# Kernel tuning notes

Measured on AMD Instinct MI355X. Metric: run time of the kernel, lower is better.

## Reference

```python
import jax, jax.numpy as jnp
import numpy as np

B = 100000          # polymers
MOLS_PER = 4        # 3 monomers + 1 solvent per polymer
N = B * MOLS_PER
D = 64              # rdkit feature dim
F = 64              # polymer-level feature dim
H = 128             # hidden dim


def setup_inputs() -> dict:
    key = jax.random.key(0)
    ks = jax.random.split(key, 6)
    polymer_feats = jax.random.normal(ks[0], (B, F), dtype=jnp.float32)
    rdkit = jax.random.normal(ks[1], (N, D), dtype=jnp.float32)
    # sorted segment ids; last molecule of each segment is the solvent
    polymer_mapping = jnp.repeat(jnp.arange(B, dtype=jnp.int32), MOLS_PER)
    W1 = jax.random.normal(ks[2], (F + 2 * D, H), dtype=jnp.float32) * 0.05
    b1 = jnp.zeros((H,), jnp.float32)
    W2 = jax.random.normal(ks[3], (H, H // 2), dtype=jnp.float32) * 0.05
    b2 = jnp.zeros((H // 2,), jnp.float32)
    W3 = jax.random.normal(ks[4], (H // 2, 1), dtype=jnp.float32) * 0.05
    b3 = jnp.zeros((1,), jnp.float32)
    return {"polymer_feats": polymer_feats, "rdkit": rdkit,
            "polymer_mapping": polymer_mapping,
            "W1": W1, "b1": b1, "W2": W2, "b2": b2, "W3": W3, "b3": b3}


def _combine_rdkit(rdkit, polymer_mapping, num_polymers):
    # solvent = last row of each consecutive segment
    last = jnp.concatenate([polymer_mapping[1:] != polymer_mapping[:-1],
                            jnp.ones((1,), dtype=bool)])
    mono = ~last
    mono_w = mono.astype(rdkit.dtype)
    mono_sum = jax.ops.segment_sum(rdkit * mono_w[:, None], polymer_mapping,
                                   num_segments=num_polymers)
    mono_cnt = jax.ops.segment_sum(mono_w, polymer_mapping,
                                   num_segments=num_polymers)
    mono_avg = mono_sum / mono_cnt[:, None]
    solvent = jax.ops.segment_sum(rdkit * last.astype(rdkit.dtype)[:, None],
                                  polymer_mapping, num_segments=num_polymers)
    return jnp.concatenate([mono_avg, solvent], axis=1)  # [B, 2D]


def reference(polymer_feats, rdkit, polymer_mapping, W1, b1, W2, b2, W3, b3):
    num_polymers = polymer_feats.shape[0]
    pooled = _combine_rdkit(rdkit, polymer_mapping, num_polymers)
    x = jnp.concatenate([polymer_feats, pooled], axis=1)  # [B, F+2D]
    h = jax.nn.relu(x @ W1 + b1)          # dropout is identity in eval mode
    h = jax.nn.relu(h @ W2 + b2)
    return h @ W3 + b3                    # [B, 1]
```

## Files before the change

kernel.cpp:

```cpp
#include <hip/hip_runtime.h>

#define BPOLY  100000
#define TILE_M 64
#define NBLK   ((BPOLY + TILE_M - 1) / TILE_M)
#define KSTR   200

typedef __attribute__((ext_vector_type(8))) _Float16 f16x8;
typedef __attribute__((ext_vector_type(4))) _Float16 f16x4;
typedef __attribute__((ext_vector_type(4))) float    f32x4;

#define W1T 0
#define W2T 24576

__global__ __launch_bounds__(256) void prep_weights(
    const float* __restrict__ W1,
    const float* __restrict__ W2,
    _Float16* __restrict__ ws) {
  int i = blockIdx.x * 256 + threadIdx.x;
  if (i < 24576) {
    int k = i >> 7, n = i & 127;
    ws[W1T + n * 192 + k] = (_Float16)W1[i];
  } else {
    int j = i - 24576;
    int k = j >> 6, n = j & 63;
    ws[W2T + n * 128 + k] = (_Float16)W2[j];
  }
}

__global__ __launch_bounds__(256, 6) void fnn_mfma(
    const float* __restrict__ pf,
    const float* __restrict__ rdkit,
    const _Float16* __restrict__ ws,
    const float* __restrict__ b1,
    const float* __restrict__ b2,
    const float* __restrict__ W3,
    const float* __restrict__ b3,
    float* __restrict__ out) {
  __shared__ __align__(16) _Float16 Xs[64 * KSTR];

  const int tid  = threadIdx.x;
  const int p0   = blockIdx.x * TILE_M;
  const int lane = tid & 63;
  const int wv   = tid >> 6;
  const int lmod = lane & 15;
  const int lq   = lane >> 4;

  #pragma unroll
  for (int i = 0; i < 4; ++i) {
    int f = tid + i * 256;
    int m = f >> 4, kq = (f & 15) * 4;
    float4 v = make_float4(0.f, 0.f, 0.f, 0.f);
    if (p0 + m < BPOLY) v = *(const float4*)(pf + (size_t)(p0 + m) * 64 + kq);
    f16x4 h = {(_Float16)v.x, (_Float16)v.y, (_Float16)v.z, (_Float16)v.w};
    *(f16x4*)&Xs[m * KSTR + kq] = h;
  }
  #pragma unroll
  for (int i = 0; i < 4; ++i) {
    int f = tid + i * 256;
    int m = f >> 4, kq = (f & 15) * 4;
    float4 r0 = {0,0,0,0}, r1 = {0,0,0,0}, r2 = {0,0,0,0}, r3 = {0,0,0,0};
    if (p0 + m < BPOLY) {
      const float* base = rdkit + (size_t)(p0 + m) * 256 + kq;
      r0 = *(const float4*)(base);
      r1 = *(const float4*)(base + 64);
      r2 = *(const float4*)(base + 128);
      r3 = *(const float4*)(base + 192);
    }
    const float inv3 = 1.0f / 3.0f;
    f16x4 av = {(_Float16)((r0.x + r1.x + r2.x) * inv3),
                (_Float16)((r0.y + r1.y + r2.y) * inv3),
                (_Float16)((r0.z + r1.z + r2.z) * inv3),
                (_Float16)((r0.w + r1.w + r2.w) * inv3)};
    f16x4 sv = {(_Float16)r3.x, (_Float16)r3.y, (_Float16)r3.z, (_Float16)r3.w};
    *(f16x4*)&Xs[m * KSTR + 64 + kq]  = av;
    *(f16x4*)&Xs[m * KSTR + 128 + kq] = sv;
  }
  __syncthreads();

  const float b1v0 = b1[32 * wv + lmod];
  const float b1v1 = b1[32 * wv + 16 + lmod];
  const _Float16* w1t = ws + W1T;
  const int bcol0 = (32 * wv + lmod) * 192;
  const int bcol1 = (32 * wv + 16 + lmod) * 192;

  f32x4 acc1[4][2];
  #pragma unroll
  for (int mt = 0; mt < 4; ++mt) {
    acc1[mt][0] = (f32x4){0.f, 0.f, 0.f, 0.f};
    acc1[mt][1] = (f32x4){0.f, 0.f, 0.f, 0.f};
  }

  #pragma unroll 2
  for (int ks = 0; ks < 6; ++ks) {
    const int ko = ks * 32 + lq * 8;
    f16x8 b0 = *(const f16x8*)(w1t + bcol0 + ko);
    f16x8 b1f = *(const f16x8*)(w1t + bcol1 + ko);
    #pragma unroll
    for (int mt = 0; mt < 4; ++mt) {
      f16x8 a = *(const f16x8*)&Xs[(mt * 16 + lmod) * KSTR + ko];
      acc1[mt][0] = __builtin_amdgcn_mfma_f32_16x16x32_f16(a, b0,  acc1[mt][0], 0, 0, 0);
      acc1[mt][1] = __builtin_amdgcn_mfma_f32_16x16x32_f16(a, b1f, acc1[mt][1], 0, 0, 0);
    }
  }
  __syncthreads();

  #pragma unroll
  for (int mt = 0; mt < 4; ++mt) {
    #pragma unroll
    for (int nn = 0; nn < 2; ++nn) {
      const float bv = nn ? b1v1 : b1v0;
      const int col = 32 * wv + 16 * nn + lmod;
      #pragma unroll
      for (int r = 0; r < 4; ++r) {
        float h = fmaxf(acc1[mt][nn][r] + bv, 0.f);
        Xs[(mt * 16 + lq * 4 + r) * KSTR + col] = (_Float16)h;
      }
    }
  }
  __syncthreads();

  const float b2v = b2[16 * wv + lmod];
  const float w3v = W3[16 * wv + lmod];
  const _Float16* w2t = ws + W2T;
  const int bcol2 = (16 * wv + lmod) * 128;

  f32x4 acc2[4];
  #pragma unroll
  for (int mt = 0; mt < 4; ++mt) acc2[mt] = (f32x4){0.f, 0.f, 0.f, 0.f};

  #pragma unroll 2
  for (int ks = 0; ks < 4; ++ks) {
    const int ko = ks * 32 + lq * 8;
    f16x8 b = *(const f16x8*)(w2t + bcol2 + ko);
    #pragma unroll
    for (int mt = 0; mt < 4; ++mt) {
      f16x8 a = *(const f16x8*)&Xs[(mt * 16 + lmod) * KSTR + ko];
      acc2[mt] = __builtin_amdgcn_mfma_f32_16x16x32_f16(a, b, acc2[mt], 0, 0, 0);
    }
  }

  float part[4][4];
  #pragma unroll
  for (int mt = 0; mt < 4; ++mt)
    #pragma unroll
    for (int r = 0; r < 4; ++r)
      part[mt][r] = fmaxf(acc2[mt][r] + b2v, 0.f) * w3v;

  #pragma unroll
  for (int mask = 1; mask <= 8; mask <<= 1)
    #pragma unroll
    for (int mt = 0; mt < 4; ++mt)
      #pragma unroll
      for (int r = 0; r < 4; ++r)
        part[mt][r] += __shfl_xor(part[mt][r], mask);

  if (lmod == 0) {
    #pragma unroll
    for (int mt = 0; mt < 4; ++mt)
      #pragma unroll
      for (int r = 0; r < 4; ++r) {
        int row = mt * 16 + lq * 4 + r;
        *(float*)&Xs[row * KSTR + 128 + 2 * wv] = part[mt][r];
      }
  }
  __syncthreads();

  if (tid < 64) {
    int p = p0 + tid;
    if (p < BPOLY) {
      float4 ps = *(const float4*)&Xs[tid * KSTR + 128];
      out[p] = ps.x + ps.y + ps.z + ps.w + b3[0];
    }
  }
}

extern "C" void kernel_launch(void* const* d_in, const int* in_sizes, int n_in,
                              void* d_out, int out_size, void* d_ws, size_t ws_size,
                              hipStream_t stream) {
  const float* pf    = (const float*)d_in[0];
  const float* rdkit = (const float*)d_in[1];
  const float* W1 = (const float*)d_in[3];
  const float* b1 = (const float*)d_in[4];
  const float* W2 = (const float*)d_in[5];
  const float* b2 = (const float*)d_in[6];
  const float* W3 = (const float*)d_in[7];
  const float* b3 = (const float*)d_in[8];
  _Float16* ws = (_Float16*)d_ws;
  float* out = (float*)d_out;

  prep_weights<<<128, 256, 0, stream>>>(W1, W2, ws);
  fnn_mfma<<<NBLK, 256, 0, stream>>>(pf, rdkit, ws, b1, b2, W3, b3, out);
}
```

Before: 195.4 us.

## Process two tiles per block and prefetch second tile during first GEMM

Each block now handles two 64-row tiles using two shared-memory buffers. The global loads for the second tile are issued into registers before the first tile's layer-1 MFMA loop and committed to LDS afterwards, so memory latency can hide behind compute. Grid size halves and occupancy hint drops from 6 to 3 blocks per CU. The cost is doubled LDS use and many more live registers, which may reduce latency hiding across waves.

```diff
diff --git a/kernel.cpp b/kernel.cpp
--- a/kernel.cpp
+++ b/kernel.cpp
@@ -2,7 +2,8 @@
 
 #define BPOLY  100000
 #define TILE_M 64
-#define NBLK   ((BPOLY + TILE_M - 1) / TILE_M)
+#define NTILE  1564
+#define NBLK   (NTILE / 2)
 #define KSTR   200
 
 typedef __attribute__((ext_vector_type(8))) _Float16 f16x8;
@@ -27,7 +28,58 @@
   }
 }
 
-__global__ __launch_bounds__(256, 6) void fnn_mfma(
+struct StagedTile {
+  float4 pfv[4];
+  float4 rk[4][4];
+};
+
+__device__ __forceinline__ void stage_issue(const float* __restrict__ pf,
+                                            const float* __restrict__ rdkit,
+                                            int p0, int tid, StagedTile& s) {
+  #pragma unroll
+  for (int i = 0; i < 4; ++i) {
+    int f = tid + i * 256, m = f >> 4, kq = (f & 15) * 4;
+    float4 z = {0.f, 0.f, 0.f, 0.f};
+    s.pfv[i] = (p0 + m < BPOLY) ? *(const float4*)(pf + (size_t)(p0 + m) * 64 + kq) : z;
+  }
+  #pragma unroll
+  for (int i = 0; i < 4; ++i) {
+    int f = tid + i * 256, m = f >> 4, kq = (f & 15) * 4;
+    float4 z = {0.f, 0.f, 0.f, 0.f};
+    const float* base = rdkit + (size_t)(p0 + m) * 256 + kq;
+    bool ok = (p0 + m < BPOLY);
+    s.rk[i][0] = ok ? *(const float4*)(base)       : z;
+    s.rk[i][1] = ok ? *(const float4*)(base + 64)  : z;
+    s.rk[i][2] = ok ? *(const float4*)(base + 128) : z;
+    s.rk[i][3] = ok ? *(const float4*)(base + 192) : z;
+  }
+}
+
+__device__ __forceinline__ void stage_commit(_Float16* __restrict__ Xs, int tid,
+                                             const StagedTile& s) {
+  #pragma unroll
+  for (int i = 0; i < 4; ++i) {
+    int f = tid + i * 256, m = f >> 4, kq = (f & 15) * 4;
+    float4 v = s.pfv[i];
+    f16x4 h = {(_Float16)v.x, (_Float16)v.y, (_Float16)v.z, (_Float16)v.w};
+    *(f16x4*)&Xs[m * KSTR + kq] = h;
+  }
+  #pragma unroll
+  for (int i = 0; i < 4; ++i) {
+    int f = tid + i * 256, m = f >> 4, kq = (f & 15) * 4;
+    float4 r0 = s.rk[i][0], r1 = s.rk[i][1], r2 = s.rk[i][2], r3 = s.rk[i][3];
+    const float inv3 = 1.0f / 3.0f;
+    f16x4 av = {(_Float16)((r0.x + r1.x + r2.x) * inv3),
+                (_Float16)((r0.y + r1.y + r2.y) * inv3),
+                (_Float16)((r0.z + r1.z + r2.z) * inv3),
+                (_Float16)((r0.w + r1.w + r2.w) * inv3)};
+    f16x4 sv = {(_Float16)r3.x, (_Float16)r3.y, (_Float16)r3.z, (_Float16)r3.w};
+    *(f16x4*)&Xs[m * KSTR + 64 + kq]  = av;
+    *(f16x4*)&Xs[m * KSTR + 128 + kq] = sv;
+  }
+}
+
+__global__ __launch_bounds__(256, 3) void fnn_mfma(
     const float* __restrict__ pf,
     const float* __restrict__ rdkit,
     const _Float16* __restrict__ ws,
@@ -36,52 +88,36 @@
     const float* __restrict__ W3,
     const float* __restrict__ b3,
     float* __restrict__ out) {
-  __shared__ __align__(16) _Float16 Xs[64 * KSTR];
+  __shared__ __align__(16) _Float16 Xs0[64 * KSTR];
+  __shared__ __align__(16) _Float16 Xs1[64 * KSTR];
 
   const int tid  = threadIdx.x;
-  const int p0   = blockIdx.x * TILE_M;
   const int lane = tid & 63;
   const int wv   = tid >> 6;
   const int lmod = lane & 15;
   const int lq   = lane >> 4;
 
-  #pragma unroll
-  for (int i = 0; i < 4; ++i) {
-    int f = tid + i * 256;
-    int m = f >> 4, kq = (f & 15) * 4;
-    float4 v = make_float4(0.f, 0.f, 0.f, 0.f);
-    if (p0 + m < BPOLY) v = *(const float4*)(pf + (size_t)(p0 + m) * 64 + kq);
-    f16x4 h = {(_Float16)v.x, (_Float16)v.y, (_Float16)v.z, (_Float16)v.w};
-    *(f16x4*)&Xs[m * KSTR + kq] = h;
-  }
-  #pragma unroll
-  for (int i = 0; i < 4; ++i) {
-    int f = tid + i * 256;
-    int m = f >> 4, kq = (f & 15) * 4;
-    float4 r0 = {0,0,0,0}, r1 = {0,0,0,0}, r2 = {0,0,0,0}, r3 = {0,0,0,0};
-    if (p0 + m < BPOLY) {
-      const float* base = rdkit + (size_t)(p0 + m) * 256 + kq;
-      r0 = *(const float4*)(base);
-      r1 = *(const float4*)(base + 64);
-      r2 = *(const float4*)(base + 128);
-      r3 = *(const float4*)(base + 192);
-    }
-    const float inv3 = 1.0f / 3.0f;
-    f16x4 av = {(_Float16)((r0.x + r1.x + r2.x) * inv3),
-                (_Float16)((r0.y + r1.y + r2.y) * inv3),
-                (_Float16)((r0.z + r1.z + r2.z) * inv3),
-                (_Float16)((r0.w + r1.w + r2.w) * inv3)};
-    f16x4 sv = {(_Float16)r3.x, (_Float16)r3.y, (_Float16)r3.z, (_Float16)r3.w};
-    *(f16x4*)&Xs[m * KSTR + 64 + kq]  = av;
-    *(f16x4*)&Xs[m * KSTR + 128 + kq] = sv;
-  }
-  __syncthreads();
+  const int p0a = (blockIdx.x * 2) * TILE_M;
+  const int p0b = (blockIdx.x * 2 + 1) * TILE_M;
 
   const float b1v0 = b1[32 * wv + lmod];
   const float b1v1 = b1[32 * wv + 16 + lmod];
+  const float b2v  = b2[16 * wv + lmod];
+  const float w3v  = W3[16 * wv + lmod];
+  const float b3v  = b3[0];
+
   const _Float16* w1t = ws + W1T;
+  const _Float16* w2t = ws + W2T;
   const int bcol0 = (32 * wv + lmod) * 192;
   const int bcol1 = (32 * wv + 16 + lmod) * 192;
+  const int bcol2 = (16 * wv + lmod) * 128;
+
+  StagedTile st;
+  stage_issue(pf, rdkit, p0a, tid, st);
+  stage_commit(Xs0, tid, st);
+  __syncthreads();
+
+  stage_issue(pf, rdkit, p0b, tid, st);
 
   f32x4 acc1[4][2];
   #pragma unroll
@@ -89,23 +125,24 @@
     acc1[mt][0] = (f32x4){0.f, 0.f, 0.f, 0.f};
     acc1[mt][1] = (f32x4){0.f, 0.f, 0.f, 0.f};
   }
-
   #pragma unroll 2
   for (int ks = 0; ks < 6; ++ks) {
     const int ko = ks * 32 + lq * 8;
-    f16x8 b0 = *(const f16x8*)(w1t + bcol0 + ko);
-    f16x8 b1f = *(const f16x8*)(w1t + bcol1 + ko);
+    f16x8 w0 = *(const f16x8*)(w1t + bcol0 + ko);
+    f16x8 w1 = *(const f16x8*)(w1t + bcol1 + ko);
     #pragma unroll
     for (int mt = 0; mt < 4; ++mt) {
-      f16x8 a = *(const f16x8*)&Xs[(mt * 16 + lmod) * KSTR + ko];
-      acc1[mt][0] = __builtin_amdgcn_mfma_f32_16x16x32_f16(a, b0,  acc1[mt][0], 0, 0, 0);
-      acc1[mt][1] = __builtin_amdgcn_mfma_f32_16x16x32_f16(a, b1f, acc1[mt][1], 0, 0, 0);
-    }
-  }
-  __syncthreads();
-
-  #pragma unroll
-  for (int mt = 0; mt < 4; ++mt) {
+      f16x8 a = *(const f16x8*)&Xs0[(mt * 16 + lmod) * KSTR + ko];
+      acc1[mt][0] = __builtin_amdgcn_mfma_f32_16x16x32_f16(a, w0, acc1[mt][0], 0, 0, 0);
+      acc1[mt][1] = __builtin_amdgcn_mfma_f32_16x16x32_f16(a, w1, acc1[mt][1], 0, 0, 0);
+    }
+  }
+
+  stage_commit(Xs1, tid, st);
+  __syncthreads();
+
+  #pragma unroll
+  for (int mt = 0; mt < 4; ++mt)
     #pragma unroll
     for (int nn = 0; nn < 2; ++nn) {
       const float bv = nn ? b1v1 : b1v0;
@@ -113,63 +150,131 @@
       #pragma unroll
       for (int r = 0; r < 4; ++r) {
         float h = fmaxf(acc1[mt][nn][r] + bv, 0.f);
-        Xs[(mt * 16 + lq * 4 + r) * KSTR + col] = (_Float16)h;
-      }
-    }
-  }
-  __syncthreads();
-
-  const float b2v = b2[16 * wv + lmod];
-  const float w3v = W3[16 * wv + lmod];
-  const _Float16* w2t = ws + W2T;
-  const int bcol2 = (16 * wv + lmod) * 128;
-
-  f32x4 acc2[4];
-  #pragma unroll
-  for (int mt = 0; mt < 4; ++mt) acc2[mt] = (f32x4){0.f, 0.f, 0.f, 0.f};
-
+        Xs0[(mt * 16 + lq * 4 + r) * KSTR + col] = (_Float16)h;
+      }
+    }
+  __syncthreads();
+
+  {
+    f32x4 acc2[4];
+    #pragma unroll
+    for (int mt = 0; mt < 4; ++mt) acc2[mt] = (f32x4){0.f, 0.f, 0.f, 0.f};
+    #pragma unroll 2
+    for (int ks = 0; ks < 4; ++ks) {
+      const int ko = ks * 32 + lq * 8;
+      f16x8 w = *(const f16x8*)(w2t + bcol2 + ko);
+      #pragma unroll
+      for (int mt = 0; mt < 4; ++mt) {
+        f16x8 a = *(const f16x8*)&Xs0[(mt * 16 + lmod) * KSTR + ko];
+        acc2[mt] = __builtin_amdgcn_mfma_f32_16x16x32_f16(a, w, acc2[mt], 0, 0, 0);
+      }
+    }
+    float part[4][4];
+    #pragma unroll
+    for (int mt = 0; mt < 4; ++mt)
+      #pragma unroll
+      for (int r = 0; r < 4; ++r)
+        part[mt][r] = fmaxf(acc2[mt][r] + b2v, 0.f) * w3v;
+    #pragma unroll
+    for (int mask = 1; mask <= 8; mask <<= 1)
+      #pragma unroll
+      for (int mt = 0; mt < 4; ++mt)
+        #pragma unroll
+        for (int r = 0; r < 4; ++r)
+          part[mt][r] += __shfl_xor(part[mt][r], mask);
+    if (lmod == 0) {
+      #pragma unroll
+      for (int mt = 0; mt < 4; ++mt)
+        #pragma unroll
+        for (int r = 0; r < 4; ++r)
+          *(float*)&Xs0[(mt * 16 + lq * 4 + r) * KSTR + 128 + 2 * wv] = part[mt][r];
+    }
+  }
+  __syncthreads();
+
+  if (tid < 64) {
+    int p = p0a + tid;
+    if (p < BPOLY) {
+      float4 ps = *(const float4*)&Xs0[tid * KSTR + 128];
+      out[p] = ps.x + ps.y + ps.z + ps.w + b3v;
+    }
+  }
+
+  #pragma unroll
+  for (int mt = 0; mt < 4; ++mt) {
+    acc1[mt][0] = (f32x4){0.f, 0.f, 0.f, 0.f};
+    acc1[mt][1] = (f32x4){0.f, 0.f, 0.f, 0.f};
+  }
   #pragma unroll 2
-  for (int ks = 0; ks < 4; ++ks) {
+  for (int ks = 0; ks < 6; ++ks) {
     const int ko = ks * 32 + lq * 8;
-    f16x8 b = *(const f16x8*)(w2t + bcol2 + ko);
+    f16x8 w0 = *(const f16x8*)(w1t + bcol0 + ko);
+    f16x8 w1 = *(const f16x8*)(w1t + bcol1 + ko);
     #pragma unroll
     for (int mt = 0; mt < 4; ++mt) {
-      f16x8 a = *(const f16x8*)&Xs[(mt * 16 + lmod) * KSTR + ko];
-      acc2[mt] = __builtin_amdgcn_mfma_f32_16x16x32_f16(a, b, acc2[mt], 0, 0, 0);
-    }
-  }
-
-  float part[4][4];
+      f16x8 a = *(const f16x8*)&Xs1[(mt * 16 + lmod) * KSTR + ko];
+      acc1[mt][0] = __builtin_amdgcn_mfma_f32_16x16x32_f16(a, w0, acc1[mt][0], 0, 0, 0);
+      acc1[mt][1] = __builtin_amdgcn_mfma_f32_16x16x32_f16(a, w1, acc1[mt][1], 0, 0, 0);
+    }
+  }
+  __syncthreads();
+
   #pragma unroll
   for (int mt = 0; mt < 4; ++mt)
     #pragma unroll
-    for (int r = 0; r < 4; ++r)
-      part[mt][r] = fmaxf(acc2[mt][r] + b2v, 0.f) * w3v;
-
-  #pragma unroll
-  for (int mask = 1; mask <= 8; mask <<= 1)
+    for (int nn = 0; nn < 2; ++nn) {
+      const float bv = nn ? b1v1 : b1v0;
+      const int col = 32 * wv + 16 * nn + lmod;
+      #pragma unroll
+      for (int r = 0; r < 4; ++r) {
+        float h = fmaxf(acc1[mt][nn][r] + bv, 0.f);
+        Xs1[(mt * 16 + lq * 4 + r) * KSTR + col] = (_Float16)h;
+      }
+    }
+  __syncthreads();
+
+  {
+    f32x4 acc2[4];
+    #pragma unroll
+    for (int mt = 0; mt < 4; ++mt) acc2[mt] = (f32x4){0.f, 0.f, 0.f, 0.f};
+    #pragma unroll 2
+    for (int ks = 0; ks < 4; ++ks) {
+      const int ko = ks * 32 + lq * 8;
+      f16x8 w = *(const f16x8*)(w2t + bcol2 + ko);
+      #pragma unroll
+      for (int mt = 0; mt < 4; ++mt) {
+        f16x8 a = *(const f16x8*)&Xs1[(mt * 16 + lmod) * KSTR + ko];
+        acc2[mt] = __builtin_amdgcn_mfma_f32_16x16x32_f16(a, w, acc2[mt], 0, 0, 0);
+      }
+    }
+    float part[4][4];
     #pragma unroll
     for (int mt = 0; mt < 4; ++mt)
       #pragma unroll
       for (int r = 0; r < 4; ++r)
-        part[mt][r] += __shfl_xor(part[mt][r], mask);
-
-  if (lmod == 0) {
-    #pragma unroll
-    for (int mt = 0; mt < 4; ++mt)
-      #pragma unroll
-      for (int r = 0; r < 4; ++r) {
-        int row = mt * 16 + lq * 4 + r;
-        *(float*)&Xs[row * KSTR + 128 + 2 * wv] = part[mt][r];
-      }
+        part[mt][r] = fmaxf(acc2[mt][r] + b2v, 0.f) * w3v;
+    #pragma unroll
+    for (int mask = 1; mask <= 8; mask <<= 1)
+      #pragma unroll
+      for (int mt = 0; mt < 4; ++mt)
+        #pragma unroll
+        for (int r = 0; r < 4; ++r)
+          part[mt][r] += __shfl_xor(part[mt][r], mask);
+    if (lmod == 0) {
+      #pragma unroll
+      for (int mt = 0; mt < 4; ++mt)
+        #pragma unroll
+        for (int r = 0; r < 4; ++r)
+          *(float*)&Xs1[(mt * 16 + lq * 4 + r) * KSTR + 128 + 2 * wv] = part[mt][r];
+    }
   }
   __syncthreads();
 
   if (tid < 64) {
-    int p = p0 + tid;
+    int p = p0b + tid;
     if (p < BPOLY) {
-      float4 ps = *(const float4*)&Xs[tid * KSTR + 128];
-      out[p] = ps.x + ps.y + ps.z + ps.w + b3[0];
+      float4 ps = *(const float4*)&Xs1[tid * KSTR + 128];
+      out[p] = ps.x + ps.y + ps.z + ps.w + b3v;
     }
   }
 }
```

Result: slower. 223.0 us (+14.1%).

## Make each wave own 16 polymers, loading A-fragments directly from global memory

Applied to the files above, without the earlier changes.

Restructures the fused MLP so each wavefront independently processes 16 polymers and computes all 128 hidden columns. A fragments are built directly in registers from global fp32 loads, with the monomer average computed in place, instead of staging a 64-row tile in shared memory. Only a small per-wave hidden buffer in LDS is kept, all block-level barriers are removed, and occupancy hints are raised. The trade-off is that each wave now reads all of W1/W2 from global or cache, giving more weight traffic per polymer, and the global loads of rdkit are less coalesced.

```diff
diff --git a/kernel.cpp b/kernel.cpp
--- a/kernel.cpp
+++ b/kernel.cpp
@@ -1,12 +1,11 @@
 #include <hip/hip_runtime.h>
 
 #define BPOLY  100000
-#define TILE_M 64
-#define NBLK   ((BPOLY + TILE_M - 1) / TILE_M)
-#define KSTR   200
+#define NWAVE  6250
+#define NBLK   1563
+#define HSTR   136
 
 typedef __attribute__((ext_vector_type(8))) _Float16 f16x8;
-typedef __attribute__((ext_vector_type(4))) _Float16 f16x4;
 typedef __attribute__((ext_vector_type(4))) float    f32x4;
 
 #define W1T 0
@@ -27,7 +26,14 @@
   }
 }
 
-__global__ __launch_bounds__(256, 6) void fnn_mfma(
+__device__ __forceinline__ f16x8 cvt8(float4 u, float4 v) {
+  f16x8 r;
+  r[0] = (_Float16)u.x; r[1] = (_Float16)u.y; r[2] = (_Float16)u.z; r[3] = (_Float16)u.w;
+  r[4] = (_Float16)v.x; r[5] = (_Float16)v.y; r[6] = (_Float16)v.z; r[7] = (_Float16)v.w;
+  return r;
+}
+
+__global__ __launch_bounds__(256, 8) void fnn_wave(
     const float* __restrict__ pf,
     const float* __restrict__ rdkit,
     const _Float16* __restrict__ ws,
@@ -36,141 +42,108 @@
     const float* __restrict__ W3,
     const float* __restrict__ b3,
     float* __restrict__ out) {
-  __shared__ __align__(16) _Float16 Xs[64 * KSTR];
+  __shared__ __align__(16) _Float16 Hs[4 * 16 * HSTR];
 
   const int tid  = threadIdx.x;
-  const int p0   = blockIdx.x * TILE_M;
+  const int wv   = tid >> 6;
   const int lane = tid & 63;
-  const int wv   = tid >> 6;
   const int lmod = lane & 15;
   const int lq   = lane >> 4;
 
+  const int p0 = (blockIdx.x * 4 + wv) * 16;
+  if (p0 >= BPOLY) return;
+  const int p = p0 + lmod;
+
+  const float4* pf4 = (const float4*)(pf + (size_t)p * 64);
+  const float4* rk4 = (const float4*)(rdkit + (size_t)p * 256);
+
+  const _Float16* w1t = ws + W1T;
+  const _Float16* w2t = ws + W2T;
+
+  f32x4 acc[8];
   #pragma unroll
-  for (int i = 0; i < 4; ++i) {
-    int f = tid + i * 256;
-    int m = f >> 4, kq = (f & 15) * 4;
-    float4 v = make_float4(0.f, 0.f, 0.f, 0.f);
-    if (p0 + m < BPOLY) v = *(const float4*)(pf + (size_t)(p0 + m) * 64 + kq);
-    f16x4 h = {(_Float16)v.x, (_Float16)v.y, (_Float16)v.z, (_Float16)v.w};
-    *(f16x4*)&Xs[m * KSTR + kq] = h;
-  }
+  for (int nt = 0; nt < 8; ++nt) acc[nt] = (f32x4){0.f, 0.f, 0.f, 0.f};
+
   #pragma unroll
-  for (int i = 0; i < 4; ++i) {
-    int f = tid + i * 256;
-    int m = f >> 4, kq = (f & 15) * 4;
-    float4 r0 = {0,0,0,0}, r1 = {0,0,0,0}, r2 = {0,0,0,0}, r3 = {0,0,0,0};
-    if (p0 + m < BPOLY) {
-      const float* base = rdkit + (size_t)(p0 + m) * 256 + kq;
-      r0 = *(const float4*)(base);
-      r1 = *(const float4*)(base + 64);
-      r2 = *(const float4*)(base + 128);
-      r3 = *(const float4*)(base + 192);
+  for (int ks = 0; ks < 6; ++ks) {
+    f16x8 a;
+    if (ks < 2) {
+      int q = ks * 8 + lq * 2;
+      a = cvt8(pf4[q], pf4[q + 1]);
+    } else if (ks < 4) {
+      int q = (ks - 2) * 8 + lq * 2;
+      float4 u0 = rk4[q],      u1 = rk4[q + 1];
+      float4 v0 = rk4[16 + q], v1 = rk4[16 + q + 1];
+      float4 w0 = rk4[32 + q], w1 = rk4[32 + q + 1];
+      const float inv3 = 1.0f / 3.0f;
+      float4 s0 = {(u0.x + v0.x + w0.x) * inv3, (u0.y + v0.y + w0.y) * inv3,
+                   (u0.z + v0.z + w0.z) * inv3, (u0.w + v0.w + w0.w) * inv3};
+      float4 s1 = {(u1.x + v1.x + w1.x) * inv3, (u1.y + v1.y + w1.y) * inv3,
+                   (u1.z + v1.z + w1.z) * inv3, (u1.w + v1.w + w1.w) * inv3};
+      a = cvt8(s0, s1);
+    } else {
+      int q = (ks - 4) * 8 + lq * 2;
+      a = cvt8(rk4[48 + q], rk4[48 + q + 1]);
     }
-    const float inv3 = 1.0f / 3.0f;
-    f16x4 av = {(_Float16)((r0.x + r1.x + r2.x) * inv3),
-                (_Float16)((r0.y + r1.y + r2.y) * inv3),
-                (_Float16)((r0.z + r1.z + r2.z) * inv3),
-                (_Float16)((r0.w + r1.w + r2.w) * inv3)};
-    f16x4 sv = {(_Float16)r3.x, (_Float16)r3.y, (_Float16)r3.z, (_Float16)r3.w};
-    *(f16x4*)&Xs[m * KSTR + 64 + kq]  = av;
-    *(f16x4*)&Xs[m * KSTR + 128 + kq] = sv;
-  }
-  __syncthreads();
-
-  const float b1v0 = b1[32 * wv + lmod];
-  const float b1v1 = b1[32 * wv + 16 + lmod];
-  const _Float16* w1t = ws + W1T;
-  const int bcol0 = (32 * wv + lmod) * 192;
-  const int bcol1 = (32 * wv + 16 + lmod) * 192;
-
-  f32x4 acc1[4][2];
-  #pragma unroll
-  for (int mt = 0; mt < 4; ++mt) {
-    acc1[mt][0] = (f32x4){0.f, 0.f, 0.f, 0.f};
-    acc1[mt][1] = (f32x4){0.f, 0.f, 0.f, 0.f};
+    const int ko = ks * 32 + lq * 8;
+    #pragma unroll
+    for (int nt = 0; nt < 8; ++nt) {
+      f16x8 b = *(const f16x8*)(w1t + (nt * 16 + lmod) * 192 + ko);
+      acc[nt] = __builtin_amdgcn_mfma_f32_16x16x32_f16(a, b, acc[nt], 0, 0, 0);
+    }
   }
 
-  #pragma unroll 2
-  for (int ks = 0; ks < 6; ++ks) {
-    const int ko = ks * 32 + lq * 8;
-    f16x8 b0 = *(const f16x8*)(w1t + bcol0 + ko);
-    f16x8 b1f = *(const f16x8*)(w1t + bcol1 + ko);
+  _Float16* hw = Hs + wv * (16 * HSTR);
+  #pragma unroll
+  for (int nt = 0; nt < 8; ++nt) {
+    float b1c = b1[nt * 16 + lmod];
     #pragma unroll
-    for (int mt = 0; mt < 4; ++mt) {
-      f16x8 a = *(const f16x8*)&Xs[(mt * 16 + lmod) * KSTR + ko];
-      acc1[mt][0] = __builtin_amdgcn_mfma_f32_16x16x32_f16(a, b0,  acc1[mt][0], 0, 0, 0);
-      acc1[mt][1] = __builtin_amdgcn_mfma_f32_16x16x32_f16(a, b1f, acc1[mt][1], 0, 0, 0);
+    for (int r = 0; r < 4; ++r) {
+      float h = fmaxf(acc[nt][r] + b1c, 0.f);
+      hw[(lq * 4 + r) * HSTR + nt * 16 + lmod] = (_Float16)h;
     }
   }
-  __syncthreads();
-
-  #pragma unroll
-  for (int mt = 0; mt < 4; ++mt) {
-    #pragma unroll
-    for (int nn = 0; nn < 2; ++nn) {
-      const float bv = nn ? b1v1 : b1v0;
-      const int col = 32 * wv + 16 * nn + lmod;
-      #pragma unroll
-      for (int r = 0; r < 4; ++r) {
-        float h = fmaxf(acc1[mt][nn][r] + bv, 0.f);
-        Xs[(mt * 16 + lq * 4 + r) * KSTR + col] = (_Float16)h;
-      }
-    }
-  }
-  __syncthreads();
-
-  const float b2v = b2[16 * wv + lmod];
-  const float w3v = W3[16 * wv + lmod];
-  const _Float16* w2t = ws + W2T;
-  const int bcol2 = (16 * wv + lmod) * 128;
+  asm volatile("s_waitcnt lgkmcnt(0)" ::: "memory");
+  __builtin_amdgcn_sched_barrier(0);
 
   f32x4 acc2[4];
   #pragma unroll
-  for (int mt = 0; mt < 4; ++mt) acc2[mt] = (f32x4){0.f, 0.f, 0.f, 0.f};
+  for (int nt = 0; nt < 4; ++nt) acc2[nt] = (f32x4){0.f, 0.f, 0.f, 0.f};
 
-  #pragma unroll 2
+  const _Float16* hrow = hw + lmod * HSTR;
+  #pragma unroll
   for (int ks = 0; ks < 4; ++ks) {
     const int ko = ks * 32 + lq * 8;
-    f16x8 b = *(const f16x8*)(w2t + bcol2 + ko);
+    f16x8 a2 = *(const f16x8*)(hrow + ko);
     #pragma unroll
-    for (int mt = 0; mt < 4; ++mt) {
-      f16x8 a = *(const f16x8*)&Xs[(mt * 16 + lmod) * KSTR + ko];
-      acc2[mt] = __builtin_amdgcn_mfma_f32_16x16x32_f16(a, b, acc2[mt], 0, 0, 0);
+    for (int nt = 0; nt < 4; ++nt) {
+      f16x8 b = *(const f16x8*)(w2t + (nt * 16 + lmod) * 128 + ko);
+      acc2[nt] = __builtin_amdgcn_mfma_f32_16x16x32_f16(a2, b, acc2[nt], 0, 0, 0);
     }
   }
 
-  float part[4][4];
+  float s0 = 0.f, s1 = 0.f, s2 = 0.f, s3 = 0.f;
   #pragma unroll
-  for (int mt = 0; mt < 4; ++mt)
-    #pragma unroll
-    for (int r = 0; r < 4; ++r)
-      part[mt][r] = fmaxf(acc2[mt][r] + b2v, 0.f) * w3v;
-
+  for (int nt = 0; nt < 4; ++nt) {
+    float b2c = b2[nt * 16 + lmod];
+    float w3c = W3[nt * 16 + lmod];
+    s0 = fmaf(fmaxf(acc2[nt][0] + b2c, 0.f), w3c, s0);
+    s1 = fmaf(fmaxf(acc2[nt][1] + b2c, 0.f), w3c, s1);
+    s2 = fmaf(fmaxf(acc2[nt][2] + b2c, 0.f), w3c, s2);
+    s3 = fmaf(fmaxf(acc2[nt][3] + b2c, 0.f), w3c, s3);
+  }
   #pragma unroll
-  for (int mask = 1; mask <= 8; mask <<= 1)
-    #pragma unroll
-    for (int mt = 0; mt < 4; ++mt)
-      #pragma unroll
-      for (int r = 0; r < 4; ++r)
-        part[mt][r] += __shfl_xor(part[mt][r], mask);
+  for (int mask = 1; mask <= 8; mask <<= 1) {
+    s0 += __shfl_xor(s0, mask);
+    s1 += __shfl_xor(s1, mask);
+    s2 += __shfl_xor(s2, mask);
+    s3 += __shfl_xor(s3, mask);
+  }
 
   if (lmod == 0) {
-    #pragma unroll
-    for (int mt = 0; mt < 4; ++mt)
-      #pragma unroll
-      for (int r = 0; r < 4; ++r) {
-        int row = mt * 16 + lq * 4 + r;
-        *(float*)&Xs[row * KSTR + 128 + 2 * wv] = part[mt][r];
-      }
-  }
-  __syncthreads();
-
-  if (tid < 64) {
-    int p = p0 + tid;
-    if (p < BPOLY) {
-      float4 ps = *(const float4*)&Xs[tid * KSTR + 128];
-      out[p] = ps.x + ps.y + ps.z + ps.w + b3[0];
-    }
+    float bb = b3[0];
+    float4 o = {s0 + bb, s1 + bb, s2 + bb, s3 + bb};
+    *(float4*)(out + p0 + lq * 4) = o;
   }
 }
 
@@ -189,5 +162,5 @@
   float* out = (float*)d_out;
 
   prep_weights<<<128, 256, 0, stream>>>(W1, W2, ws);
-  fnn_mfma<<<NBLK, 256, 0, stream>>>(pf, rdkit, ws, b1, b2, W3, b3, out);
+  fnn_wave<<<NBLK, 256, 0, stream>>>(pf, rdkit, ws, b1, b2, W3, b3, out);
 }
```

Result: slower. 234.2 us (+19.9%).

## Fold monomer averaging into W1 and feed MFMA directly from global loads

Applied to the files above, without the earlier changes.

Expands W1 to K=320 by replicating the monomer block three times, prescaled by 1/3, so the mean pooling becomes part of the first GEMM. Activations are then loaded straight from global memory into MFMA operand registers, and the LDS staging of the input tile plus one barrier are removed. This trades more MFMA work (10 k-steps instead of 6) and redundant global loads across the four waves for less LDS traffic and fewer synchronisations. Occupancy hint drops from 6 to 5 blocks.

```diff
diff --git a/kernel.cpp b/kernel.cpp
--- a/kernel.cpp
+++ b/kernel.cpp
@@ -3,31 +3,41 @@
 #define BPOLY  100000
 #define TILE_M 64
 #define NBLK   ((BPOLY + TILE_M - 1) / TILE_M)
-#define KSTR   200
+#define HSTR   136
 
 typedef __attribute__((ext_vector_type(8))) _Float16 f16x8;
-typedef __attribute__((ext_vector_type(4))) _Float16 f16x4;
 typedef __attribute__((ext_vector_type(4))) float    f32x4;
 
-#define W1T 0
-#define W2T 24576
+#define W1T2 0
+#define W2T2 40960
 
 __global__ __launch_bounds__(256) void prep_weights(
     const float* __restrict__ W1,
     const float* __restrict__ W2,
     _Float16* __restrict__ ws) {
   int i = blockIdx.x * 256 + threadIdx.x;
-  if (i < 24576) {
-    int k = i >> 7, n = i & 127;
-    ws[W1T + n * 192 + k] = (_Float16)W1[i];
+  if (i < 40960) {
+    int n = i / 320, k = i % 320;
+    float s;
+    if (k < 64)       s = W1[k * 128 + n];
+    else if (k < 256) s = W1[(64 + ((k - 64) & 63)) * 128 + n] * (1.0f / 3.0f);
+    else              s = W1[(k - 128) * 128 + n];
+    ws[W1T2 + n * 320 + k] = (_Float16)s;
   } else {
-    int j = i - 24576;
+    int j = i - 40960;
     int k = j >> 6, n = j & 63;
-    ws[W2T + n * 128 + k] = (_Float16)W2[j];
+    ws[W2T2 + n * 128 + k] = (_Float16)W2[j];
   }
 }
 
-__global__ __launch_bounds__(256, 6) void fnn_mfma(
+__device__ __forceinline__ f16x8 cvt8(float4 u, float4 v) {
+  f16x8 r;
+  r[0] = (_Float16)u.x; r[1] = (_Float16)u.y; r[2] = (_Float16)u.z; r[3] = (_Float16)u.w;
+  r[4] = (_Float16)v.x; r[5] = (_Float16)v.y; r[6] = (_Float16)v.z; r[7] = (_Float16)v.w;
+  return r;
+}
+
+__global__ __launch_bounds__(256, 5) void fnn_direct(
     const float* __restrict__ pf,
     const float* __restrict__ rdkit,
     const _Float16* __restrict__ ws,
@@ -36,52 +46,28 @@
     const float* __restrict__ W3,
     const float* __restrict__ b3,
     float* __restrict__ out) {
-  __shared__ __align__(16) _Float16 Xs[64 * KSTR];
+  __shared__ __align__(16) _Float16 Hs[64 * HSTR];
+  __shared__ float Psum[4][64];
 
   const int tid  = threadIdx.x;
-  const int p0   = blockIdx.x * TILE_M;
+  const int wv   = tid >> 6;
   const int lane = tid & 63;
-  const int wv   = tid >> 6;
   const int lmod = lane & 15;
   const int lq   = lane >> 4;
 
+  const int p0 = blockIdx.x * TILE_M;
+
+  int pm[4];
   #pragma unroll
-  for (int i = 0; i < 4; ++i) {
-    int f = tid + i * 256;
-    int m = f >> 4, kq = (f & 15) * 4;
-    float4 v = make_float4(0.f, 0.f, 0.f, 0.f);
-    if (p0 + m < BPOLY) v = *(const float4*)(pf + (size_t)(p0 + m) * 64 + kq);
-    f16x4 h = {(_Float16)v.x, (_Float16)v.y, (_Float16)v.z, (_Float16)v.w};
-    *(f16x4*)&Xs[m * KSTR + kq] = h;
+  for (int mt = 0; mt < 4; ++mt) {
+    int p = p0 + mt * 16 + lmod;
+    pm[mt] = p < BPOLY ? p : (BPOLY - 1);
   }
-  #pragma unroll
-  for (int i = 0; i < 4; ++i) {
-    int f = tid + i * 256;
-    int m = f >> 4, kq = (f & 15) * 4;
-    float4 r0 = {0,0,0,0}, r1 = {0,0,0,0}, r2 = {0,0,0,0}, r3 = {0,0,0,0};
-    if (p0 + m < BPOLY) {
-      const float* base = rdkit + (size_t)(p0 + m) * 256 + kq;
-      r0 = *(const float4*)(base);
-      r1 = *(const float4*)(base + 64);
-      r2 = *(const float4*)(base + 128);
-      r3 = *(const float4*)(base + 192);
-    }
-    const float inv3 = 1.0f / 3.0f;
-    f16x4 av = {(_Float16)((r0.x + r1.x + r2.x) * inv3),
-                (_Float16)((r0.y + r1.y + r2.y) * inv3),
-                (_Float16)((r0.z + r1.z + r2.z) * inv3),
-                (_Float16)((r0.w + r1.w + r2.w) * inv3)};
-    f16x4 sv = {(_Float16)r3.x, (_Float16)r3.y, (_Float16)r3.z, (_Float16)r3.w};
-    *(f16x4*)&Xs[m * KSTR + 64 + kq]  = av;
-    *(f16x4*)&Xs[m * KSTR + 128 + kq] = sv;
-  }
-  __syncthreads();
 
-  const float b1v0 = b1[32 * wv + lmod];
-  const float b1v1 = b1[32 * wv + 16 + lmod];
-  const _Float16* w1t = ws + W1T;
-  const int bcol0 = (32 * wv + lmod) * 192;
-  const int bcol1 = (32 * wv + 16 + lmod) * 192;
+  const _Float16* w1t = ws + W1T2;
+  const _Float16* w2t = ws + W2T2;
+  const int n0 = 32 * wv + lmod;
+  const int n1 = n0 + 16;
 
   f32x4 acc1[4][2];
   #pragma unroll
@@ -90,22 +76,34 @@
     acc1[mt][1] = (f32x4){0.f, 0.f, 0.f, 0.f};
   }
 
-  #pragma unroll 2
-  for (int ks = 0; ks < 6; ++ks) {
-    const int ko = ks * 32 + lq * 8;
-    f16x8 b0 = *(const f16x8*)(w1t + bcol0 + ko);
-    f16x8 b1f = *(const f16x8*)(w1t + bcol1 + ko);
+  #pragma unroll
+  for (int ks = 0; ks < 10; ++ks) {
+    const int reg = ks >> 1;
+    const int off = ((ks & 1) << 5) + lq * 8;
+    float4 a0[4], a1[4];
     #pragma unroll
     for (int mt = 0; mt < 4; ++mt) {
-      f16x8 a = *(const f16x8*)&Xs[(mt * 16 + lmod) * KSTR + ko];
-      acc1[mt][0] = __builtin_amdgcn_mfma_f32_16x16x32_f16(a, b0,  acc1[mt][0], 0, 0, 0);
-      acc1[mt][1] = __builtin_amdgcn_mfma_f32_16x16x32_f16(a, b1f, acc1[mt][1], 0, 0, 0);
+      const float* src = (reg == 0)
+          ? pf + (size_t)pm[mt] * 64 + off
+          : rdkit + ((size_t)pm[mt] * 4 + (reg - 1)) * 64 + off;
+      a0[mt] = *(const float4*)(src);
+      a1[mt] = *(const float4*)(src + 4);
+    }
+    const int ko = ks * 32 + lq * 8;
+    f16x8 w0 = *(const f16x8*)(w1t + n0 * 320 + ko);
+    f16x8 w1 = *(const f16x8*)(w1t + n1 * 320 + ko);
+    #pragma unroll
+    for (int mt = 0; mt < 4; ++mt) {
+      f16x8 a = cvt8(a0[mt], a1[mt]);
+      acc1[mt][0] = __builtin_amdgcn_mfma_f32_16x16x32_f16(a, w0, acc1[mt][0], 0, 0, 0);
+      acc1[mt][1] = __builtin_amdgcn_mfma_f32_16x16x32_f16(a, w1, acc1[mt][1], 0, 0, 0);
     }
   }
-  __syncthreads();
 
+  const float b1v0 = b1[n0];
+  const float b1v1 = b1[n1];
   #pragma unroll
-  for (int mt = 0; mt < 4; ++mt) {
+  for (int mt = 0; mt < 4; ++mt)
     #pragma unroll
     for (int nn = 0; nn < 2; ++nn) {
       const float bv = nn ? b1v1 : b1v0;
@@ -113,32 +111,29 @@
       #pragma unroll
       for (int r = 0; r < 4; ++r) {
         float h = fmaxf(acc1[mt][nn][r] + bv, 0.f);
-        Xs[(mt * 16 + lq * 4 + r) * KSTR + col] = (_Float16)h;
+        Hs[(mt * 16 + lq * 4 + r) * HSTR + col] = (_Float16)h;
       }
     }
-  }
   __syncthreads();
 
-  const float b2v = b2[16 * wv + lmod];
-  const float w3v = W3[16 * wv + lmod];
-  const _Float16* w2t = ws + W2T;
-  const int bcol2 = (16 * wv + lmod) * 128;
-
+  const int n2 = 16 * wv + lmod;
   f32x4 acc2[4];
   #pragma unroll
   for (int mt = 0; mt < 4; ++mt) acc2[mt] = (f32x4){0.f, 0.f, 0.f, 0.f};
 
-  #pragma unroll 2
+  #pragma unroll
   for (int ks = 0; ks < 4; ++ks) {
     const int ko = ks * 32 + lq * 8;
-    f16x8 b = *(const f16x8*)(w2t + bcol2 + ko);
+    f16x8 w = *(const f16x8*)(w2t + n2 * 128 + ko);
     #pragma unroll
     for (int mt = 0; mt < 4; ++mt) {
-      f16x8 a = *(const f16x8*)&Xs[(mt * 16 + lmod) * KSTR + ko];
-      acc2[mt] = __builtin_amdgcn_mfma_f32_16x16x32_f16(a, b, acc2[mt], 0, 0, 0);
+      f16x8 a = *(const f16x8*)&Hs[(mt * 16 + lmod) * HSTR + ko];
+      acc2[mt] = __builtin_amdgcn_mfma_f32_16x16x32_f16(a, w, acc2[mt], 0, 0, 0);
     }
   }
 
+  const float b2v = b2[n2];
+  const float w3v = W3[n2];
   float part[4][4];
   #pragma unroll
   for (int mt = 0; mt < 4; ++mt)
@@ -158,19 +153,15 @@
     #pragma unroll
     for (int mt = 0; mt < 4; ++mt)
       #pragma unroll
-      for (int r = 0; r < 4; ++r) {
-        int row = mt * 16 + lq * 4 + r;
-        *(float*)&Xs[row * KSTR + 128 + 2 * wv] = part[mt][r];
-      }
+      for (int r = 0; r < 4; ++r)
+        Psum[wv][mt * 16 + lq * 4 + r] = part[mt][r];
   }
   __syncthreads();
 
   if (tid < 64) {
     int p = p0 + tid;
-    if (p < BPOLY) {
-      float4 ps = *(const float4*)&Xs[tid * KSTR + 128];
-      out[p] = ps.x + ps.y + ps.z + ps.w + b3[0];
-    }
+    if (p < BPOLY)
+      out[p] = Psum[0][tid] + Psum[1][tid] + Psum[2][tid] + Psum[3][tid] + b3[0];
   }
 }
 
@@ -188,6 +179,6 @@
   _Float16* ws = (_Float16*)d_ws;
   float* out = (float*)d_out;
 
-  prep_weights<<<128, 256, 0, stream>>>(W1, W2, ws);
-  fnn_mfma<<<NBLK, 256, 0, stream>>>(pf, rdkit, ws, b1, b2, W3, b3, out);
+  prep_weights<<<192, 256, 0, stream>>>(W1, W2, ws);
+  fnn_direct<<<NBLK, 256, 0, stream>>>(pf, rdkit, ws, b1, b2, W3, b3, out);
 }
```

Result: slower. 230.8 us (+18.1%).
